# Performance work log

Measured on AMD Instinct MI355X. Metric: run time of the kernel, lower is better.

The kernel has to match this reference:

```python
import jax, jax.numpy as jnp
import numpy as np

B, S, DIM = 20, 500, 300          # hard-coded in the original module
HID = 600                          # expansion_factor * dim
QK = 128
ROT = 32                           # rotary dim = min(32, query_key_dim)
NB = 32                            # t5 num_buckets


def _layernorm(x, g, b, eps=1e-5):
    m = jnp.mean(x, -1, keepdims=True)
    v = jnp.var(x, -1, keepdims=True)
    return (x - m) / jnp.sqrt(v + eps) * g + b


def _silu(x):
    return x * jax.nn.sigmoid(x)


def _rotary(x):
    # rotate first ROT dims, adjacent-pair convention (rotary_embedding_torch)
    inv = 1.0 / (10000.0 ** (jnp.arange(0, ROT, 2, dtype=jnp.float32) / ROT))  # [16]
    fr = jnp.repeat(jnp.arange(S, dtype=jnp.float32)[:, None] * inv[None, :], 2, axis=-1)  # [S,32]
    cos, sin = jnp.cos(fr), jnp.sin(fr)
    xr, xp = x[..., :ROT], x[..., ROT:]
    x2 = xr.reshape(xr.shape[0], S, ROT // 2, 2)
    rot = jnp.stack([-x2[..., 1], x2[..., 0]], axis=-1).reshape(xr.shape)
    return jnp.concatenate([xr * cos + rot * sin, xp], axis=-1)


def _t5_bias(emb):
    nb = NB // 2                   # non-causal halves the buckets -> 16
    pos = jnp.arange(S)
    n = pos[:, None] - pos[None, :]  # n = -(k_pos - q_pos)
    ret = (n < 0).astype(jnp.int32) * nb
    na = jnp.abs(n)
    max_exact = nb // 2            # 8
    vil = max_exact + (jnp.log(jnp.maximum(na, 1).astype(jnp.float32) / max_exact)
                       / np.float32(np.log(128.0 / max_exact)) * (nb - max_exact)).astype(jnp.int32)
    vil = jnp.minimum(vil, nb - 1)
    bucket = ret + jnp.where(na < max_exact, na, vil)
    return emb[bucket, 0] * np.float32(QK ** 0.5)


def _gate_mask(gate):
    # Vectorized, jit-able version of the per-batch numpy threshold search.
    T = 128
    absg = jnp.abs(gate)                                   # [B,500,600]
    # histogram of floor(|g|): count(|g|>=t) for integer t via reverse cumsum
    bins = jnp.clip(jnp.floor(absg), 0, T).astype(jnp.int32)
    flat = (bins + (jnp.arange(B, dtype=jnp.int32) * (T + 1))[:, None, None]).ravel()
    hist = jnp.zeros(B * (T + 1), jnp.int32).at[flat].add(1).reshape(B, T + 1)
    cge = jnp.cumsum(hist[:, ::-1], axis=1)[:, ::-1]       # cge[:,t] = #(|g| >= t)
    gmax = jnp.floor(jnp.max(gate, axis=(1, 2)))           # loop starts at floor(max(gate))
    ts = jnp.arange(1, T + 1)
    valid = (ts[None, :] <= gmax[:, None]) & (cge[:, 1:] > 90000)  # 300000*0.3
    trim = jnp.maximum(jnp.max(jnp.where(valid, ts[None, :], 0), axis=1), 1)  # [B]
    g4 = absg.reshape(B, 100, 5, 120, 5)[:, :, :4, :, :4]
    counts = jnp.sum(g4 >= trim[:, None, None, None, None].astype(gate.dtype),
                     axis=(2, 4)).astype(jnp.int32)        # [B,100,120], <=16
    cmax = jnp.max(counts, axis=(1, 2))
    ts2 = jnp.arange(1, 17)
    c2 = jnp.sum(counts[:, :, :, None] >= ts2[None, None, None, :], axis=(1, 2))  # [B,16]
    valid2 = (ts2[None, :] <= cmax[:, None]) & (c2 > 3600)  # 12000*0.3
    found = jnp.any(valid2, axis=1)
    t2 = jnp.where(found, jnp.max(jnp.where(valid2, ts2[None, :], 0), axis=1), cmax)
    bv = jnp.where(counts >= t2[:, None, None], 1.0, 0.25).astype(gate.dtype)  # [B,100,120]
    pr = jnp.array([1.0, 1.0, 1.0, 1.0, 0.0], gate.dtype)  # 5th row/col of each block stays 0
    m = bv[:, :, None, :, None] * pr[None, None, :, None, None] * pr[None, None, None, None, :]
    return m.reshape(B, 500, 600)


def setup_inputs() -> dict:
    key = jax.random.key(0)
    ks = jax.random.split(key, 12)
    std = 0.02
    return {
        "x": jax.random.normal(ks[0], (B, S, DIM), jnp.float32),
        "my_mask2": jax.random.uniform(ks[1], (S, S), jnp.float32),
        "ln_g": jnp.ones((DIM,), jnp.float32),
        "ln_b": jnp.zeros((DIM,), jnp.float32),
        "Wh": jax.random.normal(ks[2], (DIM, 2 * HID), jnp.float32) * std,
        "bh": jnp.zeros((2 * HID,), jnp.float32),
        "Wqk": jax.random.normal(ks[3], (DIM, QK), jnp.float32) * std,
        "bqk": jnp.zeros((QK,), jnp.float32),
        "gamma": 1.0 + jax.random.normal(ks[4], (2, QK), jnp.float32) * std,
        "beta": jnp.zeros((2, QK), jnp.float32),
        "rel_emb": jax.random.normal(ks[5], (NB, 1), jnp.float32) * std,
        "Wout": jax.random.normal(ks[6], (HID, DIM), jnp.float32) * std,
        "bout": jnp.zeros((DIM,), jnp.float32),
    }


def reference(x, my_mask2, ln_g, ln_b, Wh, bh, Wqk, bqk, gamma, beta, rel_emb, Wout, bout):
    nx = _layernorm(x, ln_g, ln_b)
    xs, xp = nx[..., :DIM // 2], nx[..., DIM // 2:]
    xs = jnp.concatenate([jnp.zeros_like(xs[:, :1]), xs[:, :-1]], axis=1)  # token shift
    nx = jnp.concatenate([xs, xp], axis=-1)
    h = _silu(nx @ Wh + bh)                                 # [B,S,1200]
    v, gate = h[..., :HID], h[..., HID:]
    gm = jax.lax.stop_gradient(_gate_mask(gate))            # numpy path detaches in torch
    qk = _silu(nx @ Wqk + bqk)
    q = _rotary(qk * gamma[0] + beta[0])
    k = _rotary(qk * gamma[1] + beta[1])
    sim = jnp.einsum('bid,bjd->bij', q, k) + _t5_bias(rel_emb)[None]
    attn = jax.nn.relu(sim / S) ** 2
    attn = attn * my_mask2[None]
    out = jnp.einsum('bij,bjd->bid', attn, v)
    out = gm * out * gate
    return out @ Wout + bout + x
```

## Files before the change

### kernel.cpp

```cpp
#include <hip/hip_runtime.h>
#include <hip/hip_bf16.h>

#define BB 20
#define SS 500
#define DIMD 300
#define HIDH 600
#define QKD 128

typedef unsigned short u16;
typedef __attribute__((ext_vector_type(8))) __bf16 bf16x8;
typedef __attribute__((ext_vector_type(8))) short short8;
typedef __attribute__((ext_vector_type(4))) float floatx4;

__device__ __forceinline__ u16 f2bu(float f) {
    __hip_bfloat16 h = __float2bfloat16(f);
    return *reinterpret_cast<u16*>(&h);
}
__device__ __forceinline__ float bu2f(u16 u) {
    unsigned v = ((unsigned)u) << 16;
    return __uint_as_float(v);
}

__device__ __forceinline__ floatx4 mfma_bf16(short8 a, short8 b, floatx4 c) {
    return __builtin_amdgcn_mfma_f32_16x16x32_bf16(
        __builtin_bit_cast(bf16x8, a), __builtin_bit_cast(bf16x8, b), c, 0, 0, 0);
}

__device__ __forceinline__ void glds16(const u16* g, u16* l) {
    __builtin_amdgcn_global_load_lds(
        (__attribute__((address_space(1))) const void*)g,
        (__attribute__((address_space(3))) void*)l, 16, 0, 0);
}

__device__ __forceinline__ unsigned fenc(float m) {
    unsigned bits = __float_as_uint(m);
    return (bits & 0x80000000u) ? ~bits : (bits | 0x80000000u);
}

__global__ __launch_bounds__(256)
void prep_ln_kernel(const float* __restrict__ x, const float* __restrict__ lng,
                    const float* __restrict__ lnb, u16* __restrict__ nxb,
                    const float* __restrict__ Wh, const float* __restrict__ Wqk,
                    const float* __restrict__ Wout, const float* __restrict__ rel_emb,
                    u16* __restrict__ WhT, u16* __restrict__ Wqkb,
                    u16* __restrict__ WoutT, float* __restrict__ bias,
                    int* __restrict__ hist, unsigned* __restrict__ gmaxu,
                    int* __restrict__ h2cm) {
    long id = (long)blockIdx.x * 256 + threadIdx.x;
    if (id < 640000) {
        int bs = id >> 6;
        int t = id & 63;
        int s = bs % SS;
        const float* xr = x + (long)bs * DIMD;
        float sum = 0.f, sq = 0.f;
        for (int d = t; d < DIMD; d += 64) { float v = xr[d]; sum += v; sq += v * v; }
        for (int off = 1; off < 64; off <<= 1) {
            sum += __shfl_xor(sum, off);
            sq  += __shfl_xor(sq, off);
        }
        float mean = sum * (1.f / DIMD);
        float var  = sq * (1.f / DIMD) - mean * mean;
        float rstd = rsqrtf(var + 1e-5f);
        for (int d = t; d < DIMD; d += 64) {
            float nv = (xr[d] - mean) * rstd * lng[d] + lnb[d];
            if (d < DIMD / 2) {
                if (s < SS - 1) nxb[(long)(bs + 1) * 320 + d] = f2bu(nv);
            } else {
                nxb[(long)bs * 320 + d] = f2bu(nv);
            }
        }
        if (s == 0)
            for (int d = t; d < DIMD / 2; d += 64) nxb[(long)bs * 320 + d] = 0;
        for (int d = DIMD + t; d < 320; d += 64) nxb[(long)bs * 320 + d] = 0;
        return;
    }
    id -= 640000;
    if (id < 384000) {
        int k = id / 1200, n = id - (long)k * 1200;
        WhT[(long)n * 320 + k] = (k < 300) ? f2bu(Wh[(long)k * 1200 + n]) : (u16)0;
        return;
    }
    id -= 384000;
    if (id < 40960) {
        int k = id / 128, n = id - (long)k * 128;
        Wqkb[(long)n * 320 + k] = (k < 300) ? f2bu(Wqk[(long)k * 128 + n]) : (u16)0;
        return;
    }
    id -= 40960;
    if (id < 182400) {
        int k = id / 300, n = id - (long)k * 300;
        WoutT[(long)n * 608 + k] = (k < 600) ? f2bu(Wout[(long)k * 300 + n]) : (u16)0;
        return;
    }
    id -= 182400;
    if (id < 250000) {
        int i = id / 500, j = id - (long)i * 500;
        int n = i - j;
        int ret = (n < 0) ? 16 : 0;
        int na = n < 0 ? -n : n;
        int bucket;
        if (na < 8) bucket = ret + na;
        else {
            int vil = 8 + (int)(logf((float)na * 0.125f) / logf(16.f) * 8.f);
            vil = vil < 15 ? vil : 15;
            bucket = ret + vil;
        }
        bias[id] = rel_emb[bucket] * 11.313708498984761f;
        return;
    }
    id -= 250000;
    if (id < 5120) { hist[id] = 0; return; }
    id -= 5120;
    if (id < 1280) { gmaxu[id] = 0u; return; }
    id -= 1280;
    if (id < 1280) h2cm[(int)id] = 0;
}


struct EpiH {
    const float* bh; u16* vT; float* gateT; int* hist; unsigned* gmaxu;
    float gm0 = -1e30f, gm1 = -1e30f;
    __device__ void init(int) {}
    __device__ void operator()(float acc, int bz, int m, int n, int j) {
        if (m >= 1200 || n >= 10000) return;
        float v = acc + bh[m];
        v = v / (1.f + expf(-v));
        int b = n / SS, s = n - b * SS;
        if (m < HIDH) { vT[((long)b * 640 + m) * 512 + s] = f2bu(v); return; }
        gateT[((long)b * HIDH + (m - HIDH)) * SS + s] = v;
        if (j) gm1 = fmaxf(gm1, v); else gm0 = fmaxf(gm0, v);
        float ag = fabsf(v);
        if (ag >= 1.f) {
            int bin = (int)fminf(floorf(ag), 128.f);
            atomicAdd(&hist[b * 256 + bin], 1);
        }
    }
    __device__ void flushS(float m, int base) {
        if (base >= 10000) return;
        m = fmaxf(m, __shfl_xor(m, 16));
        m = fmaxf(m, __shfl_xor(m, 32));
        int b0 = base / SS;
        if (b0 == (base + 15) / SS) {
            m = fmaxf(m, __shfl_xor(m, 1));
            m = fmaxf(m, __shfl_xor(m, 2));
            m = fmaxf(m, __shfl_xor(m, 4));
            m = fmaxf(m, __shfl_xor(m, 8));
            if ((threadIdx.x & 63) == 0 && m > -1e29f)
                atomicMax(&gmaxu[b0 * 64], fenc(m));
        } else {
            int l = threadIdx.x & 63;
            if (l < 16 && m > -1e29f)
                atomicMax(&gmaxu[((base + l) / SS) * 64], fenc(m));
        }
    }
    __device__ void finish(int bz, int m0, int n0) {
        if (m0 + 32 <= 600) return;
        flushS(gm0, n0);
        flushS(gm1, n0 + 16);
    }
};
struct EpiQKRot {
    const float* bqk; const float* gamma; const float* beta;
    u16* qb; u16* kb;
    __device__ void init(int) const {}
    __device__ void operator()(float acc, int bz, int m, int n, int j) const {
        float v = acc + bqk[n];
        v = v / (1.f + expf(-v));
        float qp = v * gamma[n] + beta[n];
        float kp = v * gamma[QKD + n] + beta[QKD + n];
        float qx = __shfl_xor(qp, 1);
        float kx = __shfl_xor(kp, 1);
        float qo = qp, ko = kp;
        if (n < 32) {
            int s = m % SS;
            float inv = expf(-(float)(n & ~1) * (logf(10000.f) / 32.f));
            float ang = (float)s * inv;
            float c, sn;
            sincosf(ang, &sn, &c);
            float qr = (n & 1) ? qx : -qx;
            float kr = (n & 1) ? kx : -kx;
            qo = qp * c + qr * sn;
            ko = kp * c + kr * sn;
        }
        if (m < 10000) {
            qb[(long)m * QKD + n] = f2bu(qo);
            kb[(long)m * QKD + n] = f2bu(ko);
        }
    }
    __device__ void finish(int, int, int) const {}
};
struct EpiAttnB {
    const float* bias; const float* mask; u16* attnb;
    __device__ void init(int) const {}
    __device__ void operator()(float acc, int b, int m, int n, int j) const {
        if (m >= SS || n >= 512) return;
        float r = 0.f;
        if (n < SS) {
            float s = (acc + bias[m * SS + n]) * (1.f / (float)SS);
            s = fmaxf(s, 0.f);
            r = s * s * mask[m * SS + n];
        }
        attnb[((long)b * SS + m) * 512 + n] = f2bu(r);
    }
    __device__ void finish(int, int, int) const {}
};
struct EpiGateN {
    const float* gateT; const int* counts; const int* h2cm; u16* gated;
    int t2 = 0;
    __device__ void init(int b) {
        int cmax = h2cm[640 + b * 32];
        int suffix = 0, best = 0;
        bool found = false;
        for (int tt = 16; tt >= 1; --tt) {
            suffix += h2cm[b * 32 + tt];
            if (!found && tt <= cmax && suffix > 3600) { best = tt; found = true; }
        }
        t2 = found ? best : cmax;
    }
    __device__ void operator()(float acc, int b, int m, int n, int j) const {
        if (m >= SS || n >= 608) return;
        float r = 0.f;
        if (n < HIDH) {
            float g = gateT[((long)b * HIDH + n) * SS + m];
            int c = counts[(b * 100 + m / 5) * 120 + n / 5];
            float bv = (c >= t2) ? 1.f : 0.25f;
            float p = ((m % 5) == 4 || (n % 5) == 4) ? 0.f : 1.f;
            r = acc * g * bv * p;
        }
        gated[((long)(b * SS + m)) * 608 + n] = f2bu(r);
    }
    __device__ void finish(int, int, int) const {}
};
struct EpiOutB {
    const float* bout; const float* x; float* out;
    __device__ void init(int) const {}
    __device__ void operator()(float acc, int b, int m, int n, int j) const {
        if (m >= 10000 || n >= DIMD) return;
        out[(long)m * DIMD + n] = acc + bout[n] + x[(long)m * DIMD + n];
    }
    __device__ void finish(int, int, int) const {}
};

template<int MODE, class Epi>
__device__ __forceinline__ void gemm_body(
        int lin, u16* __restrict__ S,
        const u16* __restrict__ A, const u16* __restrict__ Bt,
        int Kp, int lda, int ldb, long sA, long sB,
        int TX, int TY, int bound, Epi epi) {
    int xcd = lin & 7, i = lin >> 3;
    int per = TX * TY;
    int w = i / per;
    int tl = i - w * per;
    int g = xcd + (w << 3);
    int tx = tl % TX, ty = tl / TX;
    int bx, by, bz;
    if (MODE == 0)      { if (g >= bound) return; bx = tx; by = ty; bz = g; }
    else if (MODE == 1) { bx = g * TX + tx; if (bx >= bound) return; by = ty; bz = 0; }
    else                { by = g * TY + ty; if (by >= bound) return; bx = tx; bz = 0; }

    A += (long)bz * sA; Bt += (long)bz * sB;
    int t = threadIdx.x, lane = t & 63, wave = t >> 6;
    int l15 = lane & 15, l4 = lane >> 4;
    int mw = (wave >> 1) << 5, nw = (wave & 1) << 5;
    int m0 = (by << 6) + mw;
    int n0 = (bx << 6) + nw;

    int srow = lane >> 2;
    int scol = ((lane & 3) ^ ((srow >> 1) & 3)) << 3;
    const u16* gp0;
    int drow;
    if (wave < 2) {
        gp0 = A + (long)((by << 6) + (wave << 5) + srow) * lda + scol;
        drow = wave << 5;
    } else {
        gp0 = Bt + (long)((bx << 6) + ((wave - 2) << 5) + srow) * ldb + scol;
        drow = 64 + ((wave - 2) << 5);
    }
    const u16* gp1 = gp0 + (long)16 * (wave < 2 ? lda : ldb);
    u16* d0 = S + drow * 32;
    u16* d1 = S + (drow + 16) * 32;

    floatx4 acc[2][2];
#pragma unroll
    for (int i2 = 0; i2 < 2; ++i2)
#pragma unroll
        for (int j = 0; j < 2; ++j) acc[i2][j] = (floatx4){0.f, 0.f, 0.f, 0.f};

    int nsteps = Kp >> 5;
    glds16(gp0, d0);
    glds16(gp1, d1);
    if (nsteps > 1) { glds16(gp0 + 32, d0 + 4096); glds16(gp1 + 32, d1 + 4096); }
    if (nsteps > 2) { glds16(gp0 + 64, d0 + 8192); glds16(gp1 + 64, d1 + 8192); }

    epi.init(bz);

    int rchunk = (l4 ^ ((l15 >> 1) & 3)) << 3;

    int bufc = 0;
    for (int si = 0; si < nsteps; ++si) {
        int rem = nsteps - 1 - si;
        if (rem >= 2)
            asm volatile("s_waitcnt vmcnt(4) lgkmcnt(0)" ::: "memory");
        else if (rem == 1)
            asm volatile("s_waitcnt vmcnt(2) lgkmcnt(0)" ::: "memory");
        else
            asm volatile("s_waitcnt vmcnt(0) lgkmcnt(0)" ::: "memory");
        __builtin_amdgcn_s_barrier();
        asm volatile("" ::: "memory");
        int kn = (si + 3) << 5;
        if (kn < Kp) {
            int bufp = (bufc + 3) & 3;
            glds16(gp0 + kn, d0 + bufp * 4096);
            glds16(gp1 + kn, d1 + bufp * 4096);
        }
        const u16* SB = S + bufc * 4096;
        short8 a0 = *(const short8*)(SB + ((mw + l15) << 5) + rchunk);
        short8 a1 = *(const short8*)(SB + ((mw + 16 + l15) << 5) + rchunk);
        short8 b0 = *(const short8*)(SB + ((64 + nw + l15) << 5) + rchunk);
        short8 b1 = *(const short8*)(SB + ((64 + nw + 16 + l15) << 5) + rchunk);
        acc[0][0] = mfma_bf16(a0, b0, acc[0][0]);
        acc[0][1] = mfma_bf16(a0, b1, acc[0][1]);
        acc[1][0] = mfma_bf16(a1, b0, acc[1][0]);
        acc[1][1] = mfma_bf16(a1, b1, acc[1][1]);
        bufc = (bufc + 1) & 3;
    }
#pragma unroll
    for (int i2 = 0; i2 < 2; ++i2) {
        int bm = m0 + (i2 << 4) + (l4 << 2);
#pragma unroll
        for (int j = 0; j < 2; ++j) {
            int bn = n0 + (j << 4) + l15;
#pragma unroll
            for (int r = 0; r < 4; ++r)
                epi(acc[i2][j][r], bz, bm + r, bn, j);
        }
    }
    epi.finish(bz, m0, n0);
}

template<int MODE, class Epi>
__global__ __launch_bounds__(256)
void gemm_nb(const u16* __restrict__ A, const u16* __restrict__ Bt,
             int Kp, int lda, int ldb, long sA, long sB,
             int TX, int TY, int bound, Epi epi) {
    __shared__ __align__(16) u16 S[4 * 4096];
    gemm_body<MODE>(blockIdx.x, S, A, Bt, Kp, lda, ldb, sA, sB, TX, TY, bound, epi);
}

__global__ __launch_bounds__(256)
void gemm_qk_h(const u16* __restrict__ nxb, const u16* __restrict__ Wqkb,
               const u16* __restrict__ WhT, EpiQKRot eq, EpiH eh) {
    extern __shared__ u16 S[];
    int lin = blockIdx.x;
    if (lin < 320)
        gemm_body<2>(lin, S, nxb, Wqkb, 320, 320, 320, 0L, 0L, 2, 20, 157, eq);
    else
        gemm_body<1>(lin - 320, S, WhT, nxb, 320, 320, 320, 0L, 0L, 20, 19, 157, eh);
}

__global__ __launch_bounds__(256)
void gemm_sc(const u16* __restrict__ qb, const u16* __restrict__ kb, EpiAttnB ea,
             const float* __restrict__ gateT, const int* __restrict__ hist,
             const unsigned* __restrict__ gmaxu, int* __restrict__ counts,
             int* __restrict__ h2cm) {
    extern __shared__ u16 S[];
    int lin = blockIdx.x;
    if (lin < 1536) {
        gemm_body<0>(lin, S, qb, kb, QKD, QKD, QKD,
                     (long)SS * QKD, (long)SS * QKD, 8, 8, BB, ea);
        return;
    }
    int cb = lin - 1536;
    int b = cb / 47, blk = cb - b * 47;
    int r = blk * 256 + threadIdx.x;
    int* h2l = (int*)S;
    int* smaxp = h2l + 17;
    if (threadIdx.x < 17) h2l[threadIdx.x] = 0;
    if (threadIdx.x == 0) *smaxp = 0;
    __syncthreads();
    int c = 0;
    if (r < 12000) {
        unsigned enc = gmaxu[b * 64];
        unsigned bits = (enc & 0x80000000u) ? (enc & 0x7FFFFFFFu) : ~enc;
        float gmax = floorf(__uint_as_float(bits));
        int suffix = 0, trim = 1;
        for (int tt = 128; tt >= 1; --tt) {
            suffix += hist[b * 256 + tt];
            if ((float)tt <= gmax && suffix > 90000) { trim = tt; break; }
        }
        float tr = (float)trim;
        int bi = r / 120, bj = r - bi * 120;
        const float* gb = gateT + (long)b * SS * HIDH;
#pragma unroll
        for (int cc = 0; cc < 4; ++cc)
#pragma unroll
            for (int rr = 0; rr < 4; ++rr) {
                float gv = gb[(long)(bj * 5 + cc) * SS + bi * 5 + rr];
                c += (fabsf(gv) >= tr) ? 1 : 0;
            }
        counts[b * 12000 + r] = c;
        if (c) atomicAdd(&h2l[c], 1);
    }
    int lmax = c;
    for (int off = 32; off; off >>= 1) {
        int o = __shfl_xor(lmax, off);
        lmax = lmax > o ? lmax : o;
    }
    if ((threadIdx.x & 63) == 0) atomicMax(smaxp, lmax);
    __syncthreads();
    if (threadIdx.x < 17 && h2l[threadIdx.x])
        atomicAdd(&h2cm[b * 32 + threadIdx.x], h2l[threadIdx.x]);
    if (threadIdx.x == 0) atomicMax(&h2cm[640 + b * 32], *smaxp);
}

extern "C" void kernel_launch(void* const* d_in, const int* in_sizes, int n_in,
                              void* d_out, int out_size, void* d_ws, size_t ws_size,
                              hipStream_t stream) {
    const float* x      = (const float*)d_in[0];
    const float* mask2  = (const float*)d_in[1];
    const float* ln_g   = (const float*)d_in[2];
    const float* ln_b   = (const float*)d_in[3];
    const float* Wh     = (const float*)d_in[4];
    const float* bh     = (const float*)d_in[5];
    const float* Wqk    = (const float*)d_in[6];
    const float* bqk    = (const float*)d_in[7];
    const float* gamma  = (const float*)d_in[8];
    const float* beta   = (const float*)d_in[9];
    const float* rel_emb= (const float*)d_in[10];
    const float* Wout   = (const float*)d_in[11];
    const float* bout   = (const float*)d_in[12];
    float* out = (float*)d_out;
    float* ws  = (float*)d_ws;

    float* gateT  = ws;
    float* bias   = ws + 6000000;
    u16*   nxb    = (u16*)(ws + 6250000);
    u16*   WhT    = (u16*)(ws + 7850000);
    u16*   Wqkb   = (u16*)(ws + 8042000);
    u16*   WoutT  = (u16*)(ws + 8062480);
    u16*   qb     = (u16*)(ws + 8153680);
    u16*   kb     = (u16*)(ws + 8793680);
    u16*   attnb  = (u16*)(ws + 9433680);
    u16*   vT     = (u16*)(ws + 11993680);
    u16*   gatedb = (u16*)(ws + 15270480);
    int*   hist   = (int*)(ws + 21310480);
    unsigned* gmaxu = (unsigned*)(ws + 21315600);
    int*   counts = (int*)(ws + 21316880);
    int*   h2cm   = (int*)(ws + 21556880);

    prep_ln_kernel<<<5880, 256, 0, stream>>>(x, ln_g, ln_b, nxb, Wh, Wqk, Wout,
                                             rel_emb, WhT, Wqkb, WoutT, bias,
                                             hist, gmaxu, h2cm);

    gemm_qk_h<<<3360, 256, 32768, stream>>>(
        nxb, Wqkb, WhT,
        EpiQKRot{bqk, gamma, beta, qb, kb},
        EpiH{bh, vT, gateT, hist, gmaxu});

    gemm_sc<<<2476, 256, 32768, stream>>>(
        qb, kb, EpiAttnB{bias, mask2, attnb},
        gateT, hist, gmaxu, counts, h2cm);

    gemm_nb<0><<<8 * 10 * 8 * 3, 256, 0, stream>>>(
        attnb, vT, 512, 512, 512,
        (long)SS * 512, (long)640 * 512, 10, 8, BB,
        EpiGateN{gateT, counts, h2cm, gatedb});

    gemm_nb<2><<<8 * 5 * 20, 256, 0, stream>>>(
        gatedb, WoutT, 608, 608, 608, 0L, 0L, 5, 20, 157, EpiOutB{bout, x, out});
}
```

Measured before the change: 212.4 us.

## Templatize GEMM body on per-wave register tile and buffer count, enlarge tiles

Generalizes the shared MFMA GEMM body with template parameters for per-wave M/N repeats and pipeline depth, so one block computes 128x128, 64x128 or 128x64 tiles instead of 64x64. Each A/B fragment loaded from LDS is reused across more MFMAs, and the block count drops for all four GEMMs. The gate-max epilogue is extended to four column accumulators to match. The cost is more registers and LDS per block (48KB for the 3-buffer variants), which lowers occupancy and can leave some CUs idle on these small problem sizes.

```diff
diff --git a/kernel.cpp b/kernel.cpp
--- a/kernel.cpp
+++ b/kernel.cpp
@@ -30,6 +30,15 @@
     __builtin_amdgcn_global_load_lds(
         (__attribute__((address_space(1))) const void*)g,
         (__attribute__((address_space(3))) void*)l, 16, 0, 0);
+}
+
+template<int N> __device__ __forceinline__ void vwait() {
+    if constexpr (N == 0) asm volatile("s_waitcnt vmcnt(0) lgkmcnt(0)" ::: "memory");
+    else if constexpr (N == 2) asm volatile("s_waitcnt vmcnt(2) lgkmcnt(0)" ::: "memory");
+    else if constexpr (N == 3) asm volatile("s_waitcnt vmcnt(3) lgkmcnt(0)" ::: "memory");
+    else if constexpr (N == 4) asm volatile("s_waitcnt vmcnt(4) lgkmcnt(0)" ::: "memory");
+    else if constexpr (N == 6) asm volatile("s_waitcnt vmcnt(6) lgkmcnt(0)" ::: "memory");
+    else if constexpr (N == 8) asm volatile("s_waitcnt vmcnt(8) lgkmcnt(0)" ::: "memory");
 }
 
 __device__ __forceinline__ unsigned fenc(float m) {
@@ -119,7 +128,7 @@
 
 struct EpiH {
     const float* bh; u16* vT; float* gateT; int* hist; unsigned* gmaxu;
-    float gm0 = -1e30f, gm1 = -1e30f;
+    float gm0 = -1e30f, gm1 = -1e30f, gm2 = -1e30f, gm3 = -1e30f;
     __device__ void init(int) {}
     __device__ void operator()(float acc, int bz, int m, int n, int j) {
         if (m >= 1200 || n >= 10000) return;
@@ -128,7 +137,10 @@
         int b = n / SS, s = n - b * SS;
         if (m < HIDH) { vT[((long)b * 640 + m) * 512 + s] = f2bu(v); return; }
         gateT[((long)b * HIDH + (m - HIDH)) * SS + s] = v;
-        if (j) gm1 = fmaxf(gm1, v); else gm0 = fmaxf(gm0, v);
+        if (j == 0) gm0 = fmaxf(gm0, v);
+        else if (j == 1) gm1 = fmaxf(gm1, v);
+        else if (j == 2) gm2 = fmaxf(gm2, v);
+        else gm3 = fmaxf(gm3, v);
         float ag = fabsf(v);
         if (ag >= 1.f) {
             int bin = (int)fminf(floorf(ag), 128.f);
@@ -154,9 +166,9 @@
         }
     }
     __device__ void finish(int bz, int m0, int n0) {
-        if (m0 + 32 <= 600) return;
-        flushS(gm0, n0);
-        flushS(gm1, n0 + 16);
+        if (m0 + 64 <= 600) return;
+        flushS(gm0, n0);      flushS(gm1, n0 + 16);
+        flushS(gm2, n0 + 32); flushS(gm3, n0 + 48);
     }
 };
 struct EpiQKRot {
@@ -241,12 +253,15 @@
     __device__ void finish(int, int, int) const {}
 };
 
-template<int MODE, class Epi>
+template<int MODE, int RM, int RN, int NBUF, class Epi>
 __device__ __forceinline__ void gemm_body(
         int lin, u16* __restrict__ S,
         const u16* __restrict__ A, const u16* __restrict__ Bt,
         int Kp, int lda, int ldb, long sA, long sB,
         int TX, int TY, int bound, Epi epi) {
+    constexpr int L = RM + RN;
+    constexpr int D = NBUF - 1;
+    constexpr int BUFU = 2048 * L;
     int xcd = lin & 7, i = lin >> 3;
     int per = TX * TY;
     int w = i / per;
@@ -261,36 +276,38 @@
     A += (long)bz * sA; Bt += (long)bz * sB;
     int t = threadIdx.x, lane = t & 63, wave = t >> 6;
     int l15 = lane & 15, l4 = lane >> 4;
-    int mw = (wave >> 1) << 5, nw = (wave & 1) << 5;
-    int m0 = (by << 6) + mw;
-    int n0 = (bx << 6) + nw;
+    int wr = wave >> 1, wc = wave & 1;
+    int m0 = by * (64 * RM) + wr * (32 * RM);
+    int n0 = bx * (64 * RN) + wc * (32 * RN);
 
     int srow = lane >> 2;
     int scol = ((lane & 3) ^ ((srow >> 1) & 3)) << 3;
-    const u16* gp0;
-    int drow;
-    if (wave < 2) {
-        gp0 = A + (long)((by << 6) + (wave << 5) + srow) * lda + scol;
-        drow = wave << 5;
-    } else {
-        gp0 = Bt + (long)((bx << 6) + ((wave - 2) << 5) + srow) * ldb + scol;
-        drow = 64 + ((wave - 2) << 5);
-    }
-    const u16* gp1 = gp0 + (long)16 * (wave < 2 ? lda : ldb);
-    u16* d0 = S + drow * 32;
-    u16* d1 = S + (drow + 16) * 32;
-
-    floatx4 acc[2][2];
-#pragma unroll
-    for (int i2 = 0; i2 < 2; ++i2)
-#pragma unroll
-        for (int j = 0; j < 2; ++j) acc[i2][j] = (floatx4){0.f, 0.f, 0.f, 0.f};
+    const u16* gp[L];
+    u16* dst[L];
+#pragma unroll
+    for (int q = 0; q < L; ++q) {
+        int c = wave * L + q;
+        if (c < 4 * RM)
+            gp[q] = A + (long)(by * (64 * RM) + (c << 4) + srow) * lda + scol;
+        else
+            gp[q] = Bt + (long)(bx * (64 * RN) + (((c - 4 * RM)) << 4) + srow) * ldb + scol;
+        dst[q] = S + c * 512;
+    }
+
+    floatx4 acc[2 * RM][2 * RN];
+#pragma unroll
+    for (int i2 = 0; i2 < 2 * RM; ++i2)
+#pragma unroll
+        for (int j = 0; j < 2 * RN; ++j) acc[i2][j] = (floatx4){0.f, 0.f, 0.f, 0.f};
 
     int nsteps = Kp >> 5;
-    glds16(gp0, d0);
-    glds16(gp1, d1);
-    if (nsteps > 1) { glds16(gp0 + 32, d0 + 4096); glds16(gp1 + 32, d1 + 4096); }
-    if (nsteps > 2) { glds16(gp0 + 64, d0 + 8192); glds16(gp1 + 64, d1 + 8192); }
+#pragma unroll
+    for (int pd = 0; pd < D; ++pd)
+        if (pd < nsteps) {
+#pragma unroll
+            for (int q = 0; q < L; ++q)
+                glds16(gp[q] + (pd << 5), dst[q] + pd * BUFU);
+        }
 
     epi.init(bz);
 
@@ -299,36 +316,42 @@
     int bufc = 0;
     for (int si = 0; si < nsteps; ++si) {
         int rem = nsteps - 1 - si;
-        if (rem >= 2)
-            asm volatile("s_waitcnt vmcnt(4) lgkmcnt(0)" ::: "memory");
-        else if (rem == 1)
-            asm volatile("s_waitcnt vmcnt(2) lgkmcnt(0)" ::: "memory");
-        else
-            asm volatile("s_waitcnt vmcnt(0) lgkmcnt(0)" ::: "memory");
+        if constexpr (D == 3) {
+            if (rem >= 2) vwait<2 * L>();
+            else if (rem == 1) vwait<L>();
+            else vwait<0>();
+        } else {
+            if (rem >= 1) vwait<L>();
+            else vwait<0>();
+        }
         __builtin_amdgcn_s_barrier();
         asm volatile("" ::: "memory");
-        int kn = (si + 3) << 5;
+        int kn = (si + D) << 5;
         if (kn < Kp) {
-            int bufp = (bufc + 3) & 3;
-            glds16(gp0 + kn, d0 + bufp * 4096);
-            glds16(gp1 + kn, d1 + bufp * 4096);
-        }
-        const u16* SB = S + bufc * 4096;
-        short8 a0 = *(const short8*)(SB + ((mw + l15) << 5) + rchunk);
-        short8 a1 = *(const short8*)(SB + ((mw + 16 + l15) << 5) + rchunk);
-        short8 b0 = *(const short8*)(SB + ((64 + nw + l15) << 5) + rchunk);
-        short8 b1 = *(const short8*)(SB + ((64 + nw + 16 + l15) << 5) + rchunk);
-        acc[0][0] = mfma_bf16(a0, b0, acc[0][0]);
-        acc[0][1] = mfma_bf16(a0, b1, acc[0][1]);
-        acc[1][0] = mfma_bf16(a1, b0, acc[1][0]);
-        acc[1][1] = mfma_bf16(a1, b1, acc[1][1]);
-        bufc = (bufc + 1) & 3;
-    }
-#pragma unroll
-    for (int i2 = 0; i2 < 2; ++i2) {
+            int bufp = (bufc == 0) ? NBUF - 1 : bufc - 1;
+#pragma unroll
+            for (int q = 0; q < L; ++q)
+                glds16(gp[q] + kn, dst[q] + bufp * BUFU);
+        }
+        const u16* SB = S + bufc * BUFU;
+        short8 bv[2 * RN];
+#pragma unroll
+        for (int j = 0; j < 2 * RN; ++j)
+            bv[j] = *(const short8*)(SB + ((((4 * RM + wc * 2 * RN + j) << 4) + l15) << 5) + rchunk);
+#pragma unroll
+        for (int i2 = 0; i2 < 2 * RM; ++i2) {
+            short8 av = *(const short8*)(SB + ((((wr * 2 * RM + i2) << 4) + l15) << 5) + rchunk);
+#pragma unroll
+            for (int j = 0; j < 2 * RN; ++j)
+                acc[i2][j] = mfma_bf16(av, bv[j], acc[i2][j]);
+        }
+        bufc = (bufc + 1 == NBUF) ? 0 : bufc + 1;
+    }
+#pragma unroll
+    for (int i2 = 0; i2 < 2 * RM; ++i2) {
         int bm = m0 + (i2 << 4) + (l4 << 2);
 #pragma unroll
-        for (int j = 0; j < 2; ++j) {
+        for (int j = 0; j < 2 * RN; ++j) {
             int bn = n0 + (j << 4) + l15;
 #pragma unroll
             for (int r = 0; r < 4; ++r)
@@ -338,13 +361,14 @@
     epi.finish(bz, m0, n0);
 }
 
-template<int MODE, class Epi>
+template<int MODE, int RM, int RN, int NBUF, class Epi>
 __global__ __launch_bounds__(256)
 void gemm_nb(const u16* __restrict__ A, const u16* __restrict__ Bt,
              int Kp, int lda, int ldb, long sA, long sB,
              int TX, int TY, int bound, Epi epi) {
-    __shared__ __align__(16) u16 S[4 * 4096];
-    gemm_body<MODE>(blockIdx.x, S, A, Bt, Kp, lda, ldb, sA, sB, TX, TY, bound, epi);
+    __shared__ __align__(16) u16 S[NBUF * 2048 * (RM + RN)];
+    gemm_body<MODE, RM, RN, NBUF>(blockIdx.x, S, A, Bt, Kp, lda, ldb, sA, sB,
+                                  TX, TY, bound, epi);
 }
 
 __global__ __launch_bounds__(256)
@@ -352,10 +376,12 @@
                const u16* __restrict__ WhT, EpiQKRot eq, EpiH eh) {
     extern __shared__ u16 S[];
     int lin = blockIdx.x;
-    if (lin < 320)
-        gemm_body<2>(lin, S, nxb, Wqkb, 320, 320, 320, 0L, 0L, 2, 20, 157, eq);
+    if (lin < 80)
+        gemm_body<2, 2, 2, 3>(lin, S, nxb, Wqkb, 320, 320, 320, 0L, 0L,
+                              1, 10, 79, eq);
     else
-        gemm_body<1>(lin - 320, S, WhT, nxb, 320, 320, 320, 0L, 0L, 20, 19, 157, eh);
+        gemm_body<1, 2, 2, 3>(lin - 80, S, WhT, nxb, 320, 320, 320, 0L, 0L,
+                              10, 10, 79, eh);
 }
 
 __global__ __launch_bounds__(256)
@@ -365,12 +391,12 @@
              int* __restrict__ h2cm) {
     extern __shared__ u16 S[];
     int lin = blockIdx.x;
-    if (lin < 1536) {
-        gemm_body<0>(lin, S, qb, kb, QKD, QKD, QKD,
-                     (long)SS * QKD, (long)SS * QKD, 8, 8, BB, ea);
-        return;
-    }
-    int cb = lin - 1536;
+    if (lin < 384) {
+        gemm_body<0, 2, 2, 3>(lin, S, qb, kb, QKD, QKD, QKD,
+                              (long)SS * QKD, (long)SS * QKD, 4, 4, BB, ea);
+        return;
+    }
+    int cb = lin - 384;
     int b = cb / 47, blk = cb - b * 47;
     int r = blk * 256 + threadIdx.x;
     int* h2l = (int*)S;
@@ -452,20 +478,20 @@
                                              rel_emb, WhT, Wqkb, WoutT, bias,
                                              hist, gmaxu, h2cm);
 
-    gemm_qk_h<<<3360, 256, 32768, stream>>>(
+    gemm_qk_h<<<880, 256, 49152, stream>>>(
         nxb, Wqkb, WhT,
         EpiQKRot{bqk, gamma, beta, qb, kb},
         EpiH{bh, vT, gateT, hist, gmaxu});
 
-    gemm_sc<<<2476, 256, 32768, stream>>>(
+    gemm_sc<<<1324, 256, 49152, stream>>>(
         qb, kb, EpiAttnB{bias, mask2, attnb},
         gateT, hist, gmaxu, counts, h2cm);
 
-    gemm_nb<0><<<8 * 10 * 8 * 3, 256, 0, stream>>>(
+    gemm_nb<0, 1, 2, 4><<<8 * 40 * 3, 256, 0, stream>>>(
         attnb, vT, 512, 512, 512,
-        (long)SS * 512, (long)640 * 512, 10, 8, BB,
+        (long)SS * 512, (long)640 * 512, 5, 8, BB,
         EpiGateN{gateT, counts, h2cm, gatedb});
 
-    gemm_nb<2><<<8 * 5 * 20, 256, 0, stream>>>(
-        gatedb, WoutT, 608, 608, 608, 0L, 0L, 5, 20, 157, EpiOutB{bout, x, out});
-}
+    gemm_nb<2, 2, 1, 4><<<8 * 5 * 10, 256, 0, stream>>>(
+        gatedb, WoutT, 608, 608, 608, 0L, 0L, 5, 10, 79, EpiOutB{bout, x, out});
+}
```

After: 246.7 us. 1.16x slower.
